# Kernel tuning notes

Measured on AMD Instinct MI355X. Metric: run time of the kernel, lower is better.

Reference implementation:

```python
import jax, jax.numpy as jnp
import numpy as np

HEADS = 7
DIM_HEAD = 64
SCALE = DIM_HEAD ** -0.5


def setup_inputs() -> dict:
    key = jax.random.key(0)
    ks = jax.random.split(key, 6)
    b, n, dim = 8, 1024, 448
    inner = HEADS * DIM_HEAD  # 448
    x = jax.random.normal(ks[0], (b, n, dim), dtype=jnp.float32)
    w_qv = jax.random.normal(ks[1], (dim, 2 * inner), dtype=jnp.float32) * 0.02
    ext_k = jax.random.normal(ks[2], (HEADS, n, DIM_HEAD), dtype=jnp.float32)
    ext_bias = jax.random.normal(ks[3], (HEADS, n, n), dtype=jnp.float32)
    w_out = jax.random.normal(ks[4], (inner, dim), dtype=jnp.float32) * 0.02
    b_out = jnp.zeros((dim,), dtype=jnp.float32)
    return {"x": x, "w_qv": w_qv, "ext_k": ext_k, "ext_bias": ext_bias,
            "w_out": w_out, "b_out": b_out}


def reference(x, w_qv, ext_k, ext_bias, w_out, b_out):
    b, n, dim = x.shape
    qv = x @ w_qv                                   # [b, n, 2*inner]
    q, v = jnp.split(qv, 2, axis=-1)
    # b n (h d) -> b h n d
    q = q.reshape(b, n, HEADS, DIM_HEAD).transpose(0, 2, 1, 3)
    v = v.reshape(b, n, HEADS, DIM_HEAD).transpose(0, 2, 1, 3)
    # scores vs external learned key, additive bias applied BEFORE scale
    dots = (jnp.einsum('bhnd,hmd->bhnm', q, ext_k) + ext_bias[None]) * SCALE
    attn = jax.nn.softmax(dots, axis=-1)
    out = jnp.einsum('bhnm,bhmd->bhnd', attn, v)
    out = out.transpose(0, 2, 1, 3).reshape(b, n, HEADS * DIM_HEAD)
    return out @ w_out + b_out  # dropout is identity in eval mode
```

## Files before the change

### kernel.cpp

```cpp
#include <hip/hip_runtime.h>
#include <hip/hip_bf16.h>
#include <hip/hip_fp16.h>

#define BATCH 8
#define NSEQ 1024
#define DIMM 448
#define NHEAD 7
#define HDIM 64
#define MROWS (BATCH*NSEQ)
#define KDIM 448
#define SCALE_F 0.125f
#define PSTR 66048

typedef short short8 __attribute__((ext_vector_type(8)));
typedef float floatx16 __attribute__((ext_vector_type(16)));

#define MFMA32(a,b,c) __builtin_amdgcn_mfma_f32_32x32x16_bf16(a,b,c,0,0,0)

__device__ __forceinline__ unsigned short f2bf(float f){
    __hip_bfloat16 h = __float2bfloat16(f);
    return *reinterpret_cast<unsigned short*>(&h);
}
__device__ __forceinline__ float bf2f(unsigned short u){
    __hip_bfloat16 h; *reinterpret_cast<unsigned short*>(&h) = u;
    return __bfloat162float(h);
}
__device__ __forceinline__ float h2f(unsigned short u){
    __half h; *reinterpret_cast<unsigned short*>(&h) = u;
    return __half2float(h);
}
__device__ __forceinline__ unsigned short f2h(float f){
    __half h = __float2half(f);
    return *reinterpret_cast<unsigned short*>(&h);
}

__global__ __launch_bounds__(256)
void prep_min(const float* __restrict__ x, const float* __restrict__ wqv,
              unsigned short* __restrict__ xh, unsigned short* __restrict__ wqvTh)
{
    const int bx = blockIdx.x, tid = threadIdx.x;
    if (bx < 3584) {
        int i = bx*256 + tid;
        float4 v = ((const float4*)x)[i];
        ((ushort4*)xh)[i] = make_ushort4(f2bf(v.x), f2bf(v.y), f2bf(v.z), f2bf(v.w));
    } else {
        int lid = (bx-3584)*4 + (tid>>6);
        int kc = lid % 56, ng = lid / 56;
        int n = ng*64 + (tid&63);
        unsigned short h[8];
#pragma unroll
        for (int j = 0; j < 8; ++j) h[j] = f2bf(wqv[(size_t)(kc*8+j)*896 + n]);
        size_t o = (size_t)n*KDIM + kc*8;
        *(ushort4*)(wqvTh + o)     = make_ushort4(h[0],h[1],h[2],h[3]);
        *(ushort4*)(wqvTh + o + 4) = make_ushort4(h[4],h[5],h[6],h[7]);
    }
}

__global__ __launch_bounds__(256, 2)
void gemm1_fused(const unsigned short* __restrict__ Ah, const unsigned short* __restrict__ Bh,
                 const float* __restrict__ ek, const float* __restrict__ eb,
                 const float* __restrict__ wout,
                 unsigned short* __restrict__ qd, unsigned short* __restrict__ vTd,
                 unsigned short* __restrict__ ekh, unsigned short* __restrict__ bp,
                 unsigned short* __restrict__ woTh, unsigned short* __restrict__ woTl)
{
    __shared__ float T[2][64][33];
    const int bx = blockIdx.x, tid = threadIdx.x;

    if (bx < 448) {
        const int w = tid >> 6, lane = tid & 63;
        const int lq = lane & 31, lh = lane >> 5;
        const int xb = bx & 31, y = bx >> 5;
        const int m0 = (xb*4 + w) * 64;
        const int n0 = y * 64;
        const unsigned short* aB = Ah + (size_t)(m0 + lq)*KDIM + lh*8;
        const unsigned short* bB = Bh + (size_t)(n0 + lq)*KDIM + lh*8;

        floatx16 acc[2][2] = {};
        short8 aR[2][2][2], bR[2][2][2];
#define LD1(kt, par) {                                                        \
    _Pragma("unroll") for (int fm = 0; fm < 2; ++fm)                          \
    _Pragma("unroll") for (int c = 0; c < 2; ++c) {                           \
        aR[par][fm][c] = *(const short8*)(aB + (size_t)fm*32*KDIM + (kt)*32 + c*16); \
        bR[par][fm][c] = *(const short8*)(bB + (size_t)fm*32*KDIM + (kt)*32 + c*16); } }

        LD1(0, 0)
#pragma unroll
        for (int kt = 0; kt < 14; ++kt) {
            const int par = kt & 1;
            if (kt < 13) LD1(kt+1, par^1)
#pragma unroll
            for (int c = 0; c < 2; ++c)
#pragma unroll
                for (int fm = 0; fm < 2; ++fm)
#pragma unroll
                    for (int fn = 0; fn < 2; ++fn)
                        acc[fm][fn] = MFMA32(aR[par][fm][c], bR[par][fn][c], acc[fm][fn]);
        }
#undef LD1

        if (y < NHEAD) {
#pragma unroll
            for (int fm = 0; fm < 2; ++fm)
#pragma unroll
                for (int fn = 0; fn < 2; ++fn) {
                    const int d = fn*32 + lq;
#pragma unroll
                    for (int r = 0; r < 16; ++r) {
                        const int gm = m0 + fm*32 + (r&3) + 8*(r>>2) + 4*lh;
                        const int b = gm >> 10, ns = gm & 1023;
                        qd[((size_t)((b*NHEAD + y)*NSEQ + ns))*HDIM + d] = f2bf(acc[fm][fn][r]);
                    }
                }
        } else {
            const int head = y - NHEAD;
#pragma unroll
            for (int fm = 0; fm < 2; ++fm) {
                const int gm0 = m0 + fm*32;
                const int b = gm0 >> 10, mm = (gm0 & 1023) >> 5;
                unsigned short* base = vTd + (size_t)(b*NHEAD + head)*PSTR + (size_t)mm*2048;
#pragma unroll
                for (int fn = 0; fn < 2; ++fn)
#pragma unroll
                    for (int rq = 0; rq < 4; ++rq) {
                        const int u = (rq>>1)*2 + fn;
                        const int lanep = (rq&1)*32 + lq;
                        *(ushort4*)(base + u*512 + lanep*8 + 4*lh) = make_ushort4(
                            f2bf(acc[fm][fn][rq*4+0]), f2bf(acc[fm][fn][rq*4+1]),
                            f2bf(acc[fm][fn][rq*4+2]), f2bf(acc[fm][fn][rq*4+3]));
                    }
            }
        }
    } else if (bx < 2240) {
        const int sub = tid >> 7, st = tid & 127;
        const int lid = (bx-448)*2 + sub;
        const int mt = lid & 31, qt = (lid>>5) & 15, h = lid >> 9;
#pragma unroll
        for (int it = 0; it < 4; ++it) {
            int idx = it*128 + st;
            int row = idx >> 3, c4 = (idx & 7)*4;
            float4 v = *(const float4*)(eb + ((size_t)(h*NSEQ + qt*64 + row))*NSEQ + mt*32 + c4);
            T[sub][row][c4+0]=v.x; T[sub][row][c4+1]=v.y;
            T[sub][row][c4+2]=v.z; T[sub][row][c4+3]=v.w;
        }
        __syncthreads();
        const int g2 = st >> 6, lane = st & 63;
        const int lq = lane & 31, quad = lane >> 5;
        const int q = g2*32 + lq;
        unsigned short* dst = bp + (size_t)(h*16 + qt)*PSTR
                            + (size_t)(mt*4 + g2*2)*512 + lane*8;
#pragma unroll
        for (int jj = 0; jj < 2; ++jj) {
            unsigned short o[8];
#pragma unroll
            for (int t = 0; t < 8; ++t) {
                int m = (t&3) + 8*(t>>2) + 16*jj + 4*quad;
                o[t] = f2h(T[sub][q][m] * SCALE_F);
            }
            *(ushort4*)(dst + jj*512)     = make_ushort4(o[0],o[1],o[2],o[3]);
            *(ushort4*)(dst + jj*512 + 4) = make_ushort4(o[4],o[5],o[6],o[7]);
        }
    } else if (bx < 2688) {
        int i = (bx-2240)*256 + tid;
        const int h  = i >> 14, mm = (i >> 9) & 31, c = (i >> 7) & 3;
        const int ln = (i >> 1) & 63, jh = i & 1;
        const float* src = ek + ((size_t)(h*NSEQ) + mm*32 + (ln & 31))*HDIM
                              + c*16 + (ln >> 5)*8 + jh*4;
        float4 v = *(const float4*)src;
        unsigned short* dst = ekh + (size_t)h*PSTR + (size_t)(i & 16383)*4;
        *(ushort4*)dst = make_ushort4(f2bf(v.x), f2bf(v.y), f2bf(v.z), f2bf(v.w));
    } else {
        int lid = (bx-2688)*4 + (tid>>6);
        int kc = lid % 56, ng = lid / 56;
        int n = ng*64 + (tid&63);
        ushort4 h0={0,0,0,0}, h1={0,0,0,0}, l0={0,0,0,0}, l1={0,0,0,0};
        if (n < DIMM) {
            unsigned short h[8], l[8];
#pragma unroll
            for (int j = 0; j < 8; ++j) {
                float f = wout[(size_t)(kc*8+j)*DIMM + n];
                h[j] = f2bf(f); l[j] = f2bf(f - bf2f(h[j]));
            }
            h0 = make_ushort4(h[0],h[1],h[2],h[3]); h1 = make_ushort4(h[4],h[5],h[6],h[7]);
            l0 = make_ushort4(l[0],l[1],l[2],l[3]); l1 = make_ushort4(l[4],l[5],l[6],l[7]);
        }
        size_t o = (size_t)n*KDIM + kc*8;
        *(ushort4*)(woTh + o) = h0; *(ushort4*)(woTh + o + 4) = h1;
        *(ushort4*)(woTl + o) = l0; *(ushort4*)(woTl + o + 4) = l1;
    }
}

__global__ __launch_bounds__(256, 2)
void attn7t(const unsigned short* __restrict__ qh_g, const unsigned short* __restrict__ vTh,
            const unsigned short* __restrict__ ekh, const unsigned short* __restrict__ bp,
            unsigned short* __restrict__ aoh, unsigned short* __restrict__ aol)
{
    __shared__ float linv[4][2][32];

    const int tid = threadIdx.x;
    const int w = tid >> 6, lane = tid & 63;
    const int lq = lane & 31, lh = lane >> 5;

    const int orig = blockIdx.x;
    const int wg = (orig & 7)*28 + (orig >> 3);
    const int bq = wg & 1, qt = (wg >> 1) & 15, head = wg >> 5;
    const int b = bq*4 + w;
    const int bh = b*NHEAD + head;

    short8 qf[2][4];
#pragma unroll
    for (int g2 = 0; g2 < 2; ++g2)
#pragma unroll
        for (int c = 0; c < 4; ++c)
            qf[g2][c] = *(const short8*)(qh_g +
                ((size_t)(bh*NSEQ) + qt*64 + g2*32 + lq)*HDIM + c*16 + lh*8);

    const unsigned short* kB = ekh + (size_t)head*PSTR + lane*8;
    const unsigned short* vB = vTh + (size_t)bh*PSTR + lane*8;
    const unsigned short* bB = bp + (size_t)(head*16 + qt)*PSTR + lane*8;

    short8 kR[2][4], vR[2][4], bR[2][4];
#define PREF(J, par) { const int mm = ((J) < 32) ? (J) : 0;                    \
    _Pragma("unroll") for (int c = 0; c < 4; ++c)                              \
        kR[par][c] = *(const short8*)(kB + (size_t)mm*2048 + c*512);           \
    _Pragma("unroll") for (int u = 0; u < 4; ++u)                              \
        vR[par][u] = *(const short8*)(vB + (size_t)mm*2048 + u*512);           \
    _Pragma("unroll") for (int u = 0; u < 4; ++u)                              \
        bR[par][u] = *(const short8*)(bB + (size_t)mm*2048 + u*512); }

    floatx16 O[2][2] = {};
    float ls[2] = {0.f, 0.f};

#define SEC(J, par, nxt) {                                                     \
    PREF((J)+1, nxt)                                                           \
    _Pragma("unroll") for (int g2 = 0; g2 < 2; ++g2) {                         \
        floatx16 S = {};                                                       \
        _Pragma("unroll") for (int c = 0; c < 4; ++c)                          \
            S = MFMA32(kR[par][c], qf[g2][c], S);                              \
        float pv[16];                                                          \
        _Pragma("unroll") for (int i = 0; i < 16; ++i) {                       \
            float bs = h2f((unsigned short)bR[par][g2*2 + (i>>3)][i&7]);       \
            pv[i] = __expf(fmaf(S[i], SCALE_F, bs));                           \
            ls[g2] += pv[i];                                                   \
        }                                                                      \
        unsigned wpk[8];                                                       \
        _Pragma("unroll") for (int u = 0; u < 8; ++u)                          \
            wpk[u] = (unsigned)f2bf(pv[2*u]) | ((unsigned)f2bf(pv[2*u+1]) << 16); \
        asm("v_permlane32_swap_b32 %0, %1" : "+v"(wpk[0]), "+v"(wpk[2]));      \
        asm("v_permlane32_swap_b32 %0, %1" : "+v"(wpk[1]), "+v"(wpk[3]));      \
        asm("v_permlane32_swap_b32 %0, %1" : "+v"(wpk[4]), "+v"(wpk[6]));      \
        asm("v_permlane32_swap_b32 %0, %1" : "+v"(wpk[5]), "+v"(wpk[7]));      \
        union U8 { unsigned u[4]; short8 s; };                                 \
        U8 pa0, pa1;                                                           \
        pa0.u[0]=wpk[0]; pa0.u[1]=wpk[1]; pa0.u[2]=wpk[2]; pa0.u[3]=wpk[3];    \
        pa1.u[0]=wpk[4]; pa1.u[1]=wpk[5]; pa1.u[2]=wpk[6]; pa1.u[3]=wpk[7];    \
        O[g2][0] = MFMA32(pa0.s, vR[par][0], O[g2][0]);                        \
        O[g2][1] = MFMA32(pa0.s, vR[par][1], O[g2][1]);                        \
        O[g2][0] = MFMA32(pa1.s, vR[par][2], O[g2][0]);                        \
        O[g2][1] = MFMA32(pa1.s, vR[par][3], O[g2][1]);                        \
    } }

    PREF(0, 0)
    for (int jj = 0; jj < 16; ++jj) {
        SEC(2*jj,   0, 1)
        SEC(2*jj+1, 1, 0)
    }
#undef SEC
#undef PREF

    float lt0 = ls[0] + __shfl_xor(ls[0], 32);
    float lt1 = ls[1] + __shfl_xor(ls[1], 32);
    if (lh == 0) { linv[w][0][lq] = 1.f/lt0; linv[w][1][lq] = 1.f/lt1; }

#pragma unroll
    for (int g2 = 0; g2 < 2; ++g2)
#pragma unroll
        for (int r = 0; r < 16; ++r) {
            const int qr = (r&3) + 8*(r>>2) + 4*lh;
            const float inv = linv[w][g2][qr];
            const size_t o = ((size_t)(b*NSEQ) + qt*64 + g2*32 + qr)*DIMM + head*HDIM + lq;
            float v0 = O[g2][0][r]*inv, v1 = O[g2][1][r]*inv;
            unsigned short h0 = f2bf(v0), h1 = f2bf(v1);
            aoh[o]      = h0;  aol[o]      = f2bf(v0 - bf2f(h0));
            aoh[o + 32] = h1;  aol[o + 32] = f2bf(v1 - bf2f(h1));
        }
}

__global__ __launch_bounds__(128, 2)
void gemm2_grp(const unsigned short* __restrict__ Ah, const unsigned short* __restrict__ Al,
               const unsigned short* __restrict__ Bh, const unsigned short* __restrict__ Bl,
               const float* __restrict__ bias, float* __restrict__ out)
{
    const int tid = threadIdx.x;
    const int w = tid >> 6, lane = tid & 63;
    const int lq = lane & 31, lh = lane >> 5;
    const int m0 = (blockIdx.x*2 + w) * 64;
    const int n0 = blockIdx.y * 64;
    const unsigned short* aBh = Ah + (size_t)(m0 + lq)*KDIM + lh*8;
    const unsigned short* aBl = Al + (size_t)(m0 + lq)*KDIM + lh*8;
    const unsigned short* bBh = Bh + (size_t)(n0 + lq)*KDIM + lh*8;
    const unsigned short* bBl = Bl + (size_t)(n0 + lq)*KDIM + lh*8;

    floatx16 acc[2][2] = {};
    short8 aH[2][2][2], aL[2][2][2], bH[2][2][2], bL[2][2][2];
#define LD2(kt, par) {                                                        \
    _Pragma("unroll") for (int fm = 0; fm < 2; ++fm)                          \
    _Pragma("unroll") for (int c = 0; c < 2; ++c) {                           \
        const size_t off = (size_t)fm*32*KDIM + (kt)*32 + c*16;               \
        aH[par][fm][c] = *(const short8*)(aBh + off);                         \
        aL[par][fm][c] = *(const short8*)(aBl + off);                         \
        bH[par][fm][c] = *(const short8*)(bBh + off);                         \
        bL[par][fm][c] = *(const short8*)(bBl + off); } }

    LD2(0, 0)
#pragma unroll
    for (int kt = 0; kt < 14; ++kt) {
        const int par = kt & 1;
        if (kt < 13) LD2(kt+1, par^1)
#pragma unroll
        for (int c = 0; c < 2; ++c)
#pragma unroll
            for (int fm = 0; fm < 2; ++fm)
#pragma unroll
                for (int fn = 0; fn < 2; ++fn) {
                    acc[fm][fn] = MFMA32(aH[par][fm][c], bH[par][fn][c], acc[fm][fn]);
                    acc[fm][fn] = MFMA32(aL[par][fm][c], bH[par][fn][c], acc[fm][fn]);
                    acc[fm][fn] = MFMA32(aH[par][fm][c], bL[par][fn][c], acc[fm][fn]);
                }
    }
#undef LD2

#pragma unroll
    for (int fm = 0; fm < 2; ++fm)
#pragma unroll
        for (int fn = 0; fn < 2; ++fn) {
            const int gn = n0 + fn*32 + lq;
            const float bv = bias[gn];
#pragma unroll
            for (int r = 0; r < 16; ++r) {
                const int gm = m0 + fm*32 + (r&3) + 8*(r>>2) + 4*lh;
                out[(size_t)gm*DIMM + gn] = acc[fm][fn][r] + bv;
            }
        }
}

extern "C" void kernel_launch(void* const* d_in, const int* in_sizes, int n_in,
                              void* d_out, int out_size, void* d_ws, size_t ws_size,
                              hipStream_t stream)
{
    const float* x    = (const float*)d_in[0];
    const float* wqv  = (const float*)d_in[1];
    const float* ek   = (const float*)d_in[2];
    const float* eb   = (const float*)d_in[3];
    const float* wout = (const float*)d_in[4];
    const float* bout = (const float*)d_in[5];
    float* out = (float*)d_out;

    const size_t MK = (size_t)MROWS*KDIM;
    unsigned short* p = (unsigned short*)d_ws;
    unsigned short* xh    = p;  p += MK;
    unsigned short* wqvTh = p;  p += (size_t)896*KDIM;
    unsigned short* woTh  = p;  p += (size_t)512*KDIM;
    unsigned short* woTl  = p;  p += (size_t)512*KDIM;
    unsigned short* ekh   = p;  p += (size_t)NHEAD*PSTR;
    unsigned short* qh    = p;  p += MK;
    unsigned short* vTh   = p;  p += (size_t)BATCH*NHEAD*PSTR;
    unsigned short* bp    = p;  p += (size_t)NHEAD*16*PSTR;
    unsigned short* aoh   = p;  p += MK;
    unsigned short* aol   = p;  p += MK;

    prep_min<<<3780, 256, 0, stream>>>(x, wqv, xh, wqvTh);
    gemm1_fused<<<2800, 256, 0, stream>>>(xh, wqvTh, ek, eb, wout,
                                          qh, vTh, ekh, bp, woTh, woTl);
    attn7t<<<224, 256, 0, stream>>>(qh, vTh, ekh, bp, aoh, aol);
    gemm2_grp<<<dim3(64, 7), 128, 0, stream>>>(aoh, aol, woTh, woTl, bout, out);
}
```

Measured before the change: 193.8 us.

## Split attention over key range into two halves with separate combine kernel

```diff
diff --git a/kernel.cpp b/kernel.cpp
--- a/kernel.cpp
+++ b/kernel.cpp
@@ -191,21 +191,20 @@
 }
 
 __global__ __launch_bounds__(256, 2)
-void attn7t(const unsigned short* __restrict__ qh_g, const unsigned short* __restrict__ vTh,
-            const unsigned short* __restrict__ ekh, const unsigned short* __restrict__ bp,
-            unsigned short* __restrict__ aoh, unsigned short* __restrict__ aol)
-{
-    __shared__ float linv[4][2][32];
-
+void attn_half(const unsigned short* __restrict__ qh_g, const unsigned short* __restrict__ vTh,
+               const unsigned short* __restrict__ ekh, const unsigned short* __restrict__ bp,
+               float4* __restrict__ opart, float2* __restrict__ lspart)
+{
     const int tid = threadIdx.x;
     const int w = tid >> 6, lane = tid & 63;
     const int lq = lane & 31, lh = lane >> 5;
 
     const int orig = blockIdx.x;
-    const int wg = (orig & 7)*28 + (orig >> 3);
-    const int bq = wg & 1, qt = (wg >> 1) & 15, head = wg >> 5;
+    const int wg = (orig & 7)*56 + (orig >> 3);
+    const int half = wg & 1, bq = (wg >> 1) & 1, qt = (wg >> 2) & 15, head = wg >> 6;
     const int b = bq*4 + w;
     const int bh = b*NHEAD + head;
+    const int mBeg = half*16;
 
     short8 qf[2][4];
 #pragma unroll
@@ -220,7 +219,7 @@
     const unsigned short* bB = bp + (size_t)(head*16 + qt)*PSTR + lane*8;
 
     short8 kR[2][4], vR[2][4], bR[2][4];
-#define PREF(J, par) { const int mm = ((J) < 32) ? (J) : 0;                    \
+#define PREF(J, par) { const int mm = ((J) < mBeg+16) ? (J) : mBeg;            \
     _Pragma("unroll") for (int c = 0; c < 4; ++c)                              \
         kR[par][c] = *(const short8*)(kB + (size_t)mm*2048 + c*512);           \
     _Pragma("unroll") for (int u = 0; u < 4; ++u)                              \
@@ -260,30 +259,70 @@
         O[g2][1] = MFMA32(pa1.s, vR[par][3], O[g2][1]);                        \
     } }
 
-    PREF(0, 0)
-    for (int jj = 0; jj < 16; ++jj) {
-        SEC(2*jj,   0, 1)
-        SEC(2*jj+1, 1, 0)
+    PREF(mBeg, 0)
+    for (int jj = 0; jj < 8; ++jj) {
+        SEC(mBeg+2*jj,   0, 1)
+        SEC(mBeg+2*jj+1, 1, 0)
     }
 #undef SEC
 #undef PREF
 
-    float lt0 = ls[0] + __shfl_xor(ls[0], 32);
-    float lt1 = ls[1] + __shfl_xor(ls[1], 32);
+    const int tile = (head*16 + qt)*8 + b;
+    const int wid = tile*2 + half;
+    float4* ob = opart + (size_t)wid*1024;
+#pragma unroll
+    for (int g2 = 0; g2 < 2; ++g2)
+#pragma unroll
+        for (int fn = 0; fn < 2; ++fn)
+#pragma unroll
+            for (int r4 = 0; r4 < 4; ++r4)
+                ob[((g2*2+fn)*4 + r4)*64 + lane] = make_float4(
+                    O[g2][fn][r4*4+0], O[g2][fn][r4*4+1],
+                    O[g2][fn][r4*4+2], O[g2][fn][r4*4+3]);
+    lspart[(size_t)wid*64 + lane] = make_float2(ls[0], ls[1]);
+}
+
+__global__ __launch_bounds__(256, 2)
+void attn_combine(const float4* __restrict__ opart, const float2* __restrict__ lspart,
+                  unsigned short* __restrict__ aoh, unsigned short* __restrict__ aol)
+{
+    __shared__ float linv[4][2][32];
+    const int tid = threadIdx.x;
+    const int w = tid >> 6, lane = tid & 63;
+    const int lq = lane & 31, lh = lane >> 5;
+
+    const int t = blockIdx.x*4 + w;
+    const int b = t & 7, qt = (t >> 3) & 15, head = t >> 7;
+
+    const float2 la = lspart[(size_t)(t*2)*64 + lane];
+    const float2 lb = lspart[(size_t)(t*2+1)*64 + lane];
+    float ls0 = la.x + lb.x, ls1 = la.y + lb.y;
+    float lt0 = ls0 + __shfl_xor(ls0, 32);
+    float lt1 = ls1 + __shfl_xor(ls1, 32);
     if (lh == 0) { linv[w][0][lq] = 1.f/lt0; linv[w][1][lq] = 1.f/lt1; }
 
+    const float4* oa = opart + (size_t)(t*2)*1024;
+    const float4* ob = opart + (size_t)(t*2+1)*1024;
 #pragma unroll
     for (int g2 = 0; g2 < 2; ++g2)
 #pragma unroll
-        for (int r = 0; r < 16; ++r) {
-            const int qr = (r&3) + 8*(r>>2) + 4*lh;
-            const float inv = linv[w][g2][qr];
-            const size_t o = ((size_t)(b*NSEQ) + qt*64 + g2*32 + qr)*DIMM + head*HDIM + lq;
-            float v0 = O[g2][0][r]*inv, v1 = O[g2][1][r]*inv;
-            unsigned short h0 = f2bf(v0), h1 = f2bf(v1);
-            aoh[o]      = h0;  aol[o]      = f2bf(v0 - bf2f(h0));
-            aoh[o + 32] = h1;  aol[o + 32] = f2bf(v1 - bf2f(h1));
-        }
+        for (int fn = 0; fn < 2; ++fn)
+#pragma unroll
+            for (int r4 = 0; r4 < 4; ++r4) {
+                const int ch = ((g2*2+fn)*4 + r4)*64 + lane;
+                float4 va = oa[ch], vb = ob[ch];
+                float s[4] = {va.x+vb.x, va.y+vb.y, va.z+vb.z, va.w+vb.w};
+#pragma unroll
+                for (int j = 0; j < 4; ++j) {
+                    const int qr = j + 8*r4 + 4*lh;
+                    const float inv = linv[w][g2][qr];
+                    const size_t o = ((size_t)(b*NSEQ) + qt*64 + g2*32 + qr)*DIMM
+                                   + head*HDIM + fn*32 + lq;
+                    float v = s[j]*inv;
+                    unsigned short h0 = f2bf(v);
+                    aoh[o] = h0;  aol[o] = f2bf(v - bf2f(h0));
+                }
+            }
 }
 
 __global__ __launch_bounds__(128, 2)
@@ -368,10 +407,15 @@
     unsigned short* bp    = p;  p += (size_t)NHEAD*16*PSTR;
     unsigned short* aoh   = p;  p += MK;
     unsigned short* aol   = p;  p += MK;
+    float4* opart  = (float4*)p;
+    p += (size_t)1792*1024*8;
+    float2* lspart = (float2*)p;
+    p += (size_t)1792*64*4;
 
     prep_min<<<3780, 256, 0, stream>>>(x, wqv, xh, wqvTh);
     gemm1_fused<<<2800, 256, 0, stream>>>(xh, wqvTh, ek, eb, wout,
                                           qh, vTh, ekh, bp, woTh, woTl);
-    attn7t<<<224, 256, 0, stream>>>(qh, vTh, ekh, bp, aoh, aol);
+    attn_half<<<448, 256, 0, stream>>>(qh, vTh, ekh, bp, opart, lspart);
+    attn_combine<<<224, 256, 0, stream>>>(opart, lspart, aoh, aol);
     gemm2_grp<<<dim3(64, 7), 128, 0, stream>>>(aoh, aol, woTh, woTl, bout, out);
 }
```

After: 192.7 us (median of 2 runs). No clear change (-0.6%).
